# Kernel optimization log

Measured on AMD Instinct MI355X. Metric: run time of the kernel, lower is better.

## Reference

```python
import jax, jax.numpy as jnp
import numpy as np

K = 16
D_MODEL = 128

def _gather(pts, idx):
    # pts: [B,N,C], idx: [B,N,K] -> [B,N,K,C]
    return jax.vmap(lambda p, i: p[i])(pts, idx)

def setup_inputs() -> dict:
    key = jax.random.key(0)
    ks = jax.random.split(key, 20)
    s = 0.05
    def w(k_, shape):
        return jax.random.normal(k_, shape, dtype=jnp.float32) * s
    B, N, C = 4, 4096, 3
    TF, D = 128, D_MODEL
    return {
        "xyz": jax.random.normal(ks[0], (B, N, C), dtype=jnp.float32),
        "W0a": w(ks[1], (C, TF)),  "b0a": jnp.zeros((TF,), jnp.float32),
        "W0b": w(ks[2], (TF, TF)), "b0b": jnp.zeros((TF,), jnp.float32),
        "W1":  w(ks[3], (TF, D)),  "b1":  jnp.zeros((D,), jnp.float32),
        "W2":  w(ks[4], (D, TF)),  "b2":  jnp.zeros((TF,), jnp.float32),
        "Wd1": w(ks[5], (C, D)),   "bd1": jnp.zeros((D,), jnp.float32),
        "Wd2": w(ks[6], (D, D)),   "bd2": jnp.zeros((D,), jnp.float32),
        "Wg1": w(ks[7], (D, D)),   "bg1": jnp.zeros((D,), jnp.float32),
        "Wg2": w(ks[8], (D, D)),   "bg2": jnp.zeros((D,), jnp.float32),
        "Wq":  w(ks[9], (D, D)),
        "Wk":  w(ks[10], (D, D)),
        "Wv":  w(ks[11], (D, D)),
    }

def reference(xyz, W0a, b0a, W0b, b0b, W1, b1, W2, b2,
              Wd1, bd1, Wd2, bd2, Wg1, bg1, Wg2, bg2, Wq, Wk, Wv):
    sq = jnp.sum(xyz * xyz, axis=-1)
    dists = sq[:, :, None] - 2.0 * jnp.einsum('bnc,bmc->bnm', xyz, xyz) + sq[:, None, :]
    _, knn_idx = jax.lax.top_k(-dists, K)          # [B,N,K] nearest neighbors

    knn_xyz = _gather(xyz, knn_idx)                # [B,N,K,3]
    features = jax.nn.relu(xyz @ W0a + b0a) @ W0b + b0b   # fc0  [B,N,TF]
    pre = features
    x = features @ W1 + b1                          # fc1  [B,N,D]
    q = x @ Wq                                      # [B,N,D]
    kf = _gather(x @ Wk, knn_idx)                   # [B,N,K,D]
    vf = _gather(x @ Wv, knn_idx)                   # [B,N,K,D]

    delta = xyz[:, :, None, :] - knn_xyz            # [B,N,K,3]
    pos_enc = jax.nn.relu(delta @ Wd1 + bd1) @ Wd2 + bd2   # fc_delta [B,N,K,D]

    h = q[:, :, None, :] - kf + pos_enc
    attn_logits = jax.nn.relu(h @ Wg1 + bg1) @ Wg2 + bg2   # fc_gamma [B,N,K,D]
    attn = jax.nn.softmax(attn_logits / np.sqrt(D_MODEL).astype(np.float32), axis=-2)

    res = jnp.einsum('bmnf,bmnf->bmf', attn, vf + pos_enc)  # [B,N,D]
    res = res @ W2 + b2 + pre                               # [B,N,TF]
    return res, attn
```

## Files before the change

### kernel.cpp

```cpp
#include <hip/hip_runtime.h>
#include <math.h>

#define BB 4
#define NN 4096
#define KNNK 16
#define DD 128
#define BN (BB*NN)

typedef __attribute__((ext_vector_type(8))) short short8;
typedef __attribute__((ext_vector_type(4))) float floatx4;

__device__ __forceinline__ short f2bf(float x) {
  unsigned u = __float_as_uint(x);
  unsigned r = (u + 0x7fffu + ((u >> 16) & 1u)) >> 16;
  return (short)r;
}

__device__ __forceinline__ float bf2f(short h) {
  return __uint_as_float((unsigned)(unsigned short)h << 16);
}

#define LDSFENCE() asm volatile("s_waitcnt lgkmcnt(0)" ::: "memory")

__device__ __forceinline__ void split_from_lds(const float* __restrict__ trans,
                                               int c, int g, short8 ah[4],
                                               short8 al[4]) {
#pragma unroll
  for (int s = 0; s < 4; ++s) {
    const float* p_ = &trans[c * 132 + s * 32 + g * 8];
    float4 u0 = *reinterpret_cast<const float4*>(p_);
    float4 u1 = *reinterpret_cast<const float4*>(p_ + 4);
    float tmp[8] = {u0.x, u0.y, u0.z, u0.w, u1.x, u1.y, u1.z, u1.w};
#pragma unroll
    for (int j = 0; j < 8; ++j) {
      short h_ = f2bf(tmp[j]);
      ah[s][j] = h_;
      al[s][j] = f2bf(tmp[j] - bf2f(h_));
    }
  }
}

__device__ __forceinline__ void split_gemm2(const short* __restrict__ Bh,
                                            int nt0, int lane,
                                            const short8 ah[4],
                                            const short8 al[4], floatx4& acc0,
                                            floatx4& acc1) {
  const short* Bl = Bh + 16384;
#pragma unroll
  for (int ks = 0; ks < 4; ++ks) {
    const size_t o0 = ((size_t)((nt0 + 0) * 4 + ks) * 64 + lane) * 8;
    const size_t o1 = ((size_t)((nt0 + 1) * 4 + ks) * 64 + lane) * 8;
    short8 bh0 = *reinterpret_cast<const short8*>(Bh + o0);
    short8 bl0 = *reinterpret_cast<const short8*>(Bl + o0);
    short8 bh1 = *reinterpret_cast<const short8*>(Bh + o1);
    short8 bl1 = *reinterpret_cast<const short8*>(Bl + o1);
    acc0 = __builtin_amdgcn_mfma_f32_16x16x32_bf16(ah[ks], bh0, acc0, 0, 0, 0);
    acc1 = __builtin_amdgcn_mfma_f32_16x16x32_bf16(ah[ks], bh1, acc1, 0, 0, 0);
    acc0 = __builtin_amdgcn_mfma_f32_16x16x32_bf16(ah[ks], bl0, acc0, 0, 0, 0);
    acc1 = __builtin_amdgcn_mfma_f32_16x16x32_bf16(ah[ks], bl1, acc1, 0, 0, 0);
    acc0 = __builtin_amdgcn_mfma_f32_16x16x32_bf16(al[ks], bh0, acc0, 0, 0, 0);
    acc1 = __builtin_amdgcn_mfma_f32_16x16x32_bf16(al[ks], bh1, acc1, 0, 0, 0);
  }
}

__device__ __forceinline__ void ced(double& a, double& b) {
  double mn = fmin(a, b);
  double mx = fmax(a, b);
  a = mn;
  b = mx;
}

__device__ __forceinline__ void dsort16(double v[16]) {
#define CE(i, j) ced(v[i], v[j]);
  CE(0, 1) CE(2, 3) CE(4, 5) CE(6, 7) CE(8, 9) CE(10, 11) CE(12, 13) CE(14, 15)
  CE(0, 2) CE(1, 3) CE(4, 6) CE(5, 7) CE(8, 10) CE(9, 11) CE(12, 14) CE(13, 15)
  CE(1, 2) CE(5, 6) CE(9, 10) CE(13, 14)
  CE(0, 4) CE(1, 5) CE(2, 6) CE(3, 7) CE(8, 12) CE(9, 13) CE(10, 14) CE(11, 15)
  CE(2, 4) CE(3, 5) CE(10, 12) CE(11, 13)
  CE(1, 2) CE(3, 4) CE(5, 6) CE(9, 10) CE(11, 12) CE(13, 14)
  CE(0, 8) CE(1, 9) CE(2, 10) CE(3, 11) CE(4, 12) CE(5, 13) CE(6, 14) CE(7, 15)
  CE(4, 8) CE(5, 9) CE(6, 10) CE(7, 11)
  CE(2, 4) CE(3, 5) CE(6, 8) CE(7, 9) CE(10, 12) CE(11, 13)
  CE(1, 2) CE(3, 4) CE(5, 6) CE(7, 8) CE(9, 10) CE(11, 12) CE(13, 14)
#undef CE
}

__device__ __forceinline__ void dbitonic16(double m[16]) {
#pragma unroll
  for (int s = 8; s >= 1; s >>= 1) {
#pragma unroll
    for (int i = 0; i < 16; ++i) {
      if ((i & s) == 0) ced(m[i], m[i + s]);
    }
  }
}

__global__ __launch_bounds__(256, 4) void knn_kernel(const float* __restrict__ xyz,
                                                     int* __restrict__ knn) {
  const int wv = threadIdx.x >> 6;
  const int lane = threadIdx.x & 63;
  const int q = blockIdx.x * 4 + wv;
  const int b = q >> 12;
  const int n = q & 4095;
  const float* xb = xyz + (size_t)b * NN * 3;

  const float qx = xb[n * 3 + 0], qy = xb[n * 3 + 1], qz = xb[n * 3 + 2];
  const float qsq = __fadd_rn(__fadd_rn(__fmul_rn(qx, qx), __fmul_rn(qy, qy)),
                              __fmul_rn(qz, qz));

  double top[16];
#pragma unroll
  for (int batch = 0; batch < 4; ++batch) {
    double v[16];
#pragma unroll
    for (int i = 0; i < 16; ++i) {
      const int c = (batch * 16 + i) * 64 + lane;
      float cx = xb[c * 3 + 0], cy = xb[c * 3 + 1], cz = xb[c * 3 + 2];
      float csq = __fadd_rn(__fadd_rn(__fmul_rn(cx, cx), __fmul_rn(cy, cy)),
                            __fmul_rn(cz, cz));
      float dot = __fadd_rn(__fadd_rn(__fmul_rn(qx, cx), __fmul_rn(qy, cy)),
                            __fmul_rn(qz, cz));
      float d = __fadd_rn(__fsub_rn(qsq, __fmul_rn(2.0f, dot)), csq);
      unsigned u = __float_as_uint(d);
      u = (u & 0x80000000u) ? ~u : (u | 0x80000000u);
      unsigned long long key =
          0x3FF0000000000000ULL | (((unsigned long long)u << 12) | (unsigned)c);
      v[i] = __longlong_as_double((long long)key);
    }
    dsort16(v);
    if (batch == 0) {
#pragma unroll
      for (int i = 0; i < 16; ++i) top[i] = v[i];
    } else {
      double m[16];
#pragma unroll
      for (int i = 0; i < 16; ++i)
        m[i] = fmin(top[i], v[15 - i]);
      dbitonic16(m);
#pragma unroll
      for (int i = 0; i < 16; ++i) top[i] = m[i];
    }
  }

#pragma unroll
  for (int mask = 1; mask <= 32; mask <<= 1) {
    double oth[16];
#pragma unroll
    for (int i = 0; i < 16; ++i) {
      double y = __shfl_xor(top[15 - i], mask);
      oth[i] = fmin(y, top[i]);
    }
    dbitonic16(oth);
#pragma unroll
    for (int i = 0; i < 16; ++i) top[i] = oth[i];
  }

  if (lane == 0) {
    int* outp = knn + (size_t)q * KNNK;
#pragma unroll
    for (int k = 0; k < 16; ++k)
      outp[k] = (int)(__double_as_longlong(top[k]) & 0xFFFLL);
  }
}

__global__ void swz_all_kernel(const float* __restrict__ Wd2,
                               const float* __restrict__ Wg1,
                               const float* __restrict__ Wg2,
                               const float* __restrict__ W0b,
                               const float* __restrict__ W1,
                               const float* __restrict__ Wq,
                               const float* __restrict__ Wk,
                               const float* __restrict__ Wv,
                               const float* __restrict__ W2,
                               short* __restrict__ wsw,
                               short* __restrict__ wsplit) {
  int t = blockIdx.x * 256 + threadIdx.x;
  if (t < 3 * 2048) {
    int stage = t / 2048;
    int rem = t % 2048;
    int nt = rem / 256;
    int ks = (rem % 256) / 64;
    int lane = rem % 64;
    const float* W = (stage == 0) ? Wd2 : (stage == 1) ? Wg1 : Wg2;
    short8 o;
#pragma unroll
    for (int j = 0; j < 8; ++j) {
      int k = ks * 32 + (lane >> 4) * 8 + j;
      int n = nt * 16 + (lane & 15);
      o[j] = f2bf(W[k * 128 + n]);
    }
    *reinterpret_cast<short8*>(wsw + (size_t)t * 8) = o;
  } else {
    int u = t - 3 * 2048;
    if (u >= 6 * 2048) return;
    int mat = u / 2048;
    int rem = u % 2048;
    int nt = rem / 256;
    int ks = (rem % 256) / 64;
    int lane = rem % 64;
    const float* W = (mat == 0) ? W0b : (mat == 1) ? W1 : (mat == 2) ? Wq
                     : (mat == 3) ? Wk : (mat == 4) ? Wv : W2;
    short8 hi, lo;
#pragma unroll
    for (int j = 0; j < 8; ++j) {
      int k = ks * 32 + (lane >> 4) * 8 + j;
      int n = nt * 16 + (lane & 15);
      float w = W[k * 128 + n];
      short h = f2bf(w);
      hi[j] = h;
      lo[j] = f2bf(w - bf2f(h));
    }
    *reinterpret_cast<short8*>(wsplit + ((size_t)(2 * mat) * 2048 + rem) * 8) = hi;
    *reinterpret_cast<short8*>(wsplit + ((size_t)(2 * mat + 1) * 2048 + rem) * 8) = lo;
  }
}

__global__ __launch_bounds__(256, 4) void point_mlp_mfma_kernel(
    const float* __restrict__ xyz, const float* __restrict__ W0a,
    const float* __restrict__ b0a, const float* __restrict__ b0b,
    const float* __restrict__ b1, const short* __restrict__ wsplit,
    float* __restrict__ pre, float* __restrict__ qv, float* __restrict__ kv,
    float* __restrict__ vv) {
  const int wv = threadIdx.x >> 6;
  const int lane = threadIdx.x & 63;
  const int g = lane >> 4;
  const int c = lane & 15;
  const int g0 = blockIdx.x * 16;
  const int nt0 = wv * 2;

  __shared__ __attribute__((aligned(16))) float trans[16 * 132];
  __shared__ float xs[64];
  if (threadIdx.x < 48) {
    int p = threadIdx.x / 3, cc = threadIdx.x % 3;
    xs[p * 4 + cc] = xyz[(size_t)(g0 + p) * 3 + cc];
  }
  __syncthreads();

  short8 ah[4], al[4];
  {
    const float x0 = xs[c * 4 + 0], x1 = xs[c * 4 + 1], x2 = xs[c * 4 + 2];
#pragma unroll
    for (int s = 0; s < 4; ++s) {
#pragma unroll
      for (int j = 0; j < 8; ++j) {
        const int k = s * 32 + g * 8 + j;
        float v = fmaf(x2, W0a[256 + k],
                       fmaf(x1, W0a[128 + k], fmaf(x0, W0a[k], b0a[k])));
        v = fmaxf(v, 0.f);
        const short h = f2bf(v);
        ah[s][j] = h;
        al[s][j] = f2bf(v - bf2f(h));
      }
    }
  }

  floatx4 acc0, acc1;
  const floatx4 zf = (floatx4){0.f, 0.f, 0.f, 0.f};

  acc0 = zf; acc1 = zf;
  split_gemm2(wsplit + 0 * 32768, nt0, lane, ah, al, acc0, acc1);
  {
    const float bb0 = b0b[nt0 * 16 + c];
    const float bb1 = b0b[(nt0 + 1) * 16 + c];
#pragma unroll
    for (int r = 0; r < 4; ++r) {
      const int row = g * 4 + r;
      float v0 = acc0[r] + bb0;
      float v1 = acc1[r] + bb1;
      pre[(size_t)(g0 + row) * 128 + nt0 * 16 + c] = v0;
      pre[(size_t)(g0 + row) * 128 + (nt0 + 1) * 16 + c] = v1;
      trans[row * 132 + nt0 * 16 + c] = v0;
      trans[row * 132 + (nt0 + 1) * 16 + c] = v1;
    }
  }
  __syncthreads();
  split_from_lds(trans, c, g, ah, al);
  __syncthreads();

  acc0 = zf; acc1 = zf;
  split_gemm2(wsplit + 1 * 32768, nt0, lane, ah, al, acc0, acc1);
  {
    const float bb0 = b1[nt0 * 16 + c];
    const float bb1 = b1[(nt0 + 1) * 16 + c];
#pragma unroll
    for (int r = 0; r < 4; ++r) {
      const int row = g * 4 + r;
      trans[row * 132 + nt0 * 16 + c] = acc0[r] + bb0;
      trans[row * 132 + (nt0 + 1) * 16 + c] = acc1[r] + bb1;
    }
  }
  __syncthreads();
  split_from_lds(trans, c, g, ah, al);
  __syncthreads();

#define GSTORE(dst)                                                            \
  _Pragma("unroll") for (int r = 0; r < 4; ++r) {                              \
    const int row = g0 + g * 4 + r;                                            \
    dst[(size_t)row * 128 + nt0 * 16 + c] = acc0[r];                           \
    dst[(size_t)row * 128 + (nt0 + 1) * 16 + c] = acc1[r];                     \
  }

  acc0 = zf; acc1 = zf;
  split_gemm2(wsplit + 2 * 32768, nt0, lane, ah, al, acc0, acc1);
  GSTORE(qv);

  acc0 = zf; acc1 = zf;
  split_gemm2(wsplit + 3 * 32768, nt0, lane, ah, al, acc0, acc1);
  GSTORE(kv);

  acc0 = zf; acc1 = zf;
  split_gemm2(wsplit + 4 * 32768, nt0, lane, ah, al, acc0, acc1);
  GSTORE(vv);

#undef GSTORE
}

__device__ __forceinline__ void wstage(const short* __restrict__ wsw_stage,
                                       short* __restrict__ wlds, int wv,
                                       int lane) {
#pragma unroll
  for (int i = 0; i < 8; ++i) {
    short8 w_ = *reinterpret_cast<const short8*>(wsw_stage + wv * 4096 +
                                                 i * 512 + lane * 8);
    *reinterpret_cast<short8*>(&wlds[wv * 4096 + i * 512 + lane * 8]) = w_;
  }
}

__global__ __launch_bounds__(256, 3) void attn_mfma_kernel(
    const float* __restrict__ xyz, const int* __restrict__ knn,
    const float* __restrict__ qv, const float* __restrict__ kv,
    const float* __restrict__ vv, const short* __restrict__ wsw,
    const float* __restrict__ Wd1, const float* __restrict__ bd1,
    const float* __restrict__ bd2, const float* __restrict__ bg1,
    const float* __restrict__ bg2, float* __restrict__ res_ws,
    float* __restrict__ out_attn) {
  const int wv = threadIdx.x >> 6;
  const int lane = threadIdx.x & 63;
  const int g = lane >> 4;
  const int c = lane & 15;
  const int bn = blockIdx.x * 4 + wv;
  const int b = bn >> 12;
  const int base_n = b << 12;

  __shared__ __attribute__((aligned(16))) short wlds[16384];
  __shared__ __attribute__((aligned(16))) short conv[4][16 * 136];

  const int* knnp = knn + (size_t)bn * 16;
  const int idxn = knnp[c];
  int idxr[4];
#pragma unroll
  for (int r = 0; r < 4; ++r) idxr[r] = knnp[g * 4 + r];

  float kvf[8][4];
#pragma unroll
  for (int nt = 0; nt < 8; ++nt)
#pragma unroll
    for (int r = 0; r < 4; ++r)
      kvf[nt][r] = kv[((size_t)(base_n + idxr[r])) * 128 + nt * 16 + c];

  const float ddx = xyz[(size_t)bn * 3 + 0] - xyz[((size_t)(base_n + idxn)) * 3 + 0];
  const float ddy = xyz[(size_t)bn * 3 + 1] - xyz[((size_t)(base_n + idxn)) * 3 + 1];
  const float ddz = xyz[(size_t)bn * 3 + 2] - xyz[((size_t)(base_n + idxn)) * 3 + 2];

  short8 af[4];
#pragma unroll
  for (int s = 0; s < 4; ++s) {
#pragma unroll
    for (int j = 0; j < 8; ++j) {
      int d = s * 32 + g * 8 + j;
      float v = fmaf(ddz, Wd1[256 + d],
                     fmaf(ddy, Wd1[128 + d], fmaf(ddx, Wd1[d], bd1[d])));
      af[s][j] = f2bf(fmaxf(v, 0.f));
    }
  }

  float qc[8], bd2v[8];
#pragma unroll
  for (int nt = 0; nt < 8; ++nt) {
    qc[nt] = qv[(size_t)bn * 128 + nt * 16 + c];
    bd2v[nt] = bd2[nt * 16 + c];
  }

  floatx4 acc[8];

#define STAGE_GEMM_LDS()                                                       \
  {                                                                            \
    _Pragma("unroll") for (int ks = 0; ks < 4; ++ks) {                         \
      _Pragma("unroll") for (int h2 = 0; h2 < 2; ++h2) {                       \
        short8 bfr[4];                                                         \
        _Pragma("unroll") for (int i = 0; i < 4; ++i)                          \
          bfr[i] = *reinterpret_cast<const short8*>(                           \
              &wlds[((h2 * 4 + i) * 4 + ks) * 512 + lane * 8]);                \
        _Pragma("unroll") for (int i = 0; i < 4; ++i)                          \
          acc[h2 * 4 + i] = __builtin_amdgcn_mfma_f32_16x16x32_bf16(           \
              af[ks], bfr[i], acc[h2 * 4 + i], 0, 0, 0);                       \
      }                                                                        \
    }                                                                          \
  }

  wstage(wsw, wlds, wv, lane);
  __syncthreads();
#pragma unroll
  for (int nt = 0; nt < 8; ++nt) acc[nt] = (floatx4){0.f, 0.f, 0.f, 0.f};
  STAGE_GEMM_LDS();

  float PE[8][4];
#pragma unroll
  for (int nt = 0; nt < 8; ++nt) {
#pragma unroll
    for (int r = 0; r < 4; ++r) {
      float pe = acc[nt][r] + bd2v[nt];
      PE[nt][r] = pe;
      conv[wv][(g * 4 + r) * 136 + nt * 16 + c] =
          f2bf(qc[nt] - kvf[nt][r] + pe);
    }
  }
  LDSFENCE();
#pragma unroll
  for (int s = 0; s < 4; ++s)
    af[s] = *reinterpret_cast<const short8*>(&conv[wv][c * 136 + s * 32 + g * 8]);

  __syncthreads();
  wstage(wsw + 16384, wlds, wv, lane);
  __syncthreads();
#pragma unroll
  for (int nt = 0; nt < 8; ++nt) acc[nt] = (floatx4){0.f, 0.f, 0.f, 0.f};
  STAGE_GEMM_LDS();
#pragma unroll
  for (int nt = 0; nt < 8; ++nt) {
    const float bg1v = bg1[nt * 16 + c];
#pragma unroll
    for (int r = 0; r < 4; ++r) {
      conv[wv][(g * 4 + r) * 136 + nt * 16 + c] =
          f2bf(fmaxf(acc[nt][r] + bg1v, 0.f));
    }
  }
  LDSFENCE();
#pragma unroll
  for (int s = 0; s < 4; ++s)
    af[s] = *reinterpret_cast<const short8*>(&conv[wv][c * 136 + s * 32 + g * 8]);

  __syncthreads();
  wstage(wsw + 32768, wlds, wv, lane);
  __syncthreads();

  const float inv = 0.0883883476483184f;
  float resv[8];
#pragma unroll
  for (int h = 0; h < 2; ++h) {
    const int ntb = h * 4;
    float vvf[4][4];
#pragma unroll
    for (int i = 0; i < 4; ++i)
#pragma unroll
      for (int r = 0; r < 4; ++r)
        vvf[i][r] =
            vv[((size_t)(base_n + idxr[r])) * 128 + (ntb + i) * 16 + c];

    floatx4 acch[4];
#pragma unroll
    for (int i = 0; i < 4; ++i) acch[i] = (floatx4){0.f, 0.f, 0.f, 0.f};
#pragma unroll
    for (int ks = 0; ks < 4; ++ks) {
      short8 bfr[4];
#pragma unroll
      for (int i = 0; i < 4; ++i)
        bfr[i] = *reinterpret_cast<const short8*>(
            &wlds[((ntb + i) * 4 + ks) * 512 + lane * 8]);
#pragma unroll
      for (int i = 0; i < 4; ++i)
        acch[i] = __builtin_amdgcn_mfma_f32_16x16x32_bf16(af[ks], bfr[i],
                                                          acch[i], 0, 0, 0);
    }

#pragma unroll
    for (int i = 0; i < 4; ++i) {
      const int nt = ntb + i;
      const float bg2v = bg2[nt * 16 + c];
      float l0 = (acch[i][0] + bg2v) * inv;
      float l1 = (acch[i][1] + bg2v) * inv;
      float l2 = (acch[i][2] + bg2v) * inv;
      float l3 = (acch[i][3] + bg2v) * inv;
      float m4 = fmaxf(fmaxf(l0, l1), fmaxf(l2, l3));
      m4 = fmaxf(m4, __shfl_xor(m4, 16));
      m4 = fmaxf(m4, __shfl_xor(m4, 32));
      float e0 = expf(l0 - m4), e1 = expf(l1 - m4);
      float e2 = expf(l2 - m4), e3 = expf(l3 - m4);
      float s4 = e0 + e1 + e2 + e3;
      s4 += __shfl_xor(s4, 16);
      s4 += __shfl_xor(s4, 32);
      float rs = 1.f / s4;
      float a0 = e0 * rs, a1 = e1 * rs, a2 = e2 * rs, a3 = e3 * rs;
      size_t base = ((size_t)bn * 16 + g * 4) * 128 + nt * 16 + c;
      out_attn[base + 0 * 128] = a0;
      out_attn[base + 1 * 128] = a1;
      out_attn[base + 2 * 128] = a2;
      out_attn[base + 3 * 128] = a3;
      float r = 0.f;
      r = fmaf(a0, vvf[i][0] + PE[nt][0], r);
      r = fmaf(a1, vvf[i][1] + PE[nt][1], r);
      r = fmaf(a2, vvf[i][2] + PE[nt][2], r);
      r = fmaf(a3, vvf[i][3] + PE[nt][3], r);
      r += __shfl_xor(r, 16);
      r += __shfl_xor(r, 32);
      resv[nt] = r;
    }
  }
#undef STAGE_GEMM_LDS

  if (g == 0) {
#pragma unroll
    for (int nt = 0; nt < 8; ++nt)
      res_ws[(size_t)bn * 128 + nt * 16 + c] = resv[nt];
  }
}

__global__ __launch_bounds__(256, 4) void epilogue_mfma_kernel(
    const float* __restrict__ res_ws, const short* __restrict__ wsplit,
    const float* __restrict__ b2, const float* __restrict__ pre,
    float* __restrict__ out_res) {
  const int wv = threadIdx.x >> 6;
  const int lane = threadIdx.x & 63;
  const int g = lane >> 4;
  const int c = lane & 15;
  const int g0 = blockIdx.x * 16;
  const int nt0 = wv * 2;

  __shared__ __attribute__((aligned(16))) float trans[16 * 132];

#pragma unroll
  for (int i = 0; i < 2; ++i) {
    int idx4 = threadIdx.x + i * 256;
    int row = idx4 >> 5;
    int col4 = idx4 & 31;
    float4 v = *reinterpret_cast<const float4*>(
        res_ws + (size_t)(g0 + row) * 128 + col4 * 4);
    *reinterpret_cast<float4*>(&trans[row * 132 + col4 * 4]) = v;
  }
  __syncthreads();

  short8 ah[4], al[4];
  split_from_lds(trans, c, g, ah, al);

  float prv0[4], prv1[4];
  const float bb0 = b2[nt0 * 16 + c];
  const float bb1 = b2[(nt0 + 1) * 16 + c];
#pragma unroll
  for (int r = 0; r < 4; ++r) {
    prv0[r] = pre[(size_t)(g0 + g * 4 + r) * 128 + nt0 * 16 + c];
    prv1[r] = pre[(size_t)(g0 + g * 4 + r) * 128 + (nt0 + 1) * 16 + c];
  }

  floatx4 acc0 = (floatx4){0.f, 0.f, 0.f, 0.f};
  floatx4 acc1 = (floatx4){0.f, 0.f, 0.f, 0.f};
  split_gemm2(wsplit + 5 * 32768, nt0, lane, ah, al, acc0, acc1);

#pragma unroll
  for (int r = 0; r < 4; ++r) {
    const int row = g0 + g * 4 + r;
    out_res[(size_t)row * 128 + nt0 * 16 + c] = acc0[r] + bb0 + prv0[r];
    out_res[(size_t)row * 128 + (nt0 + 1) * 16 + c] = acc1[r] + bb1 + prv1[r];
  }
}

extern "C" void kernel_launch(void* const* d_in, const int* in_sizes, int n_in,
                              void* d_out, int out_size, void* d_ws,
                              size_t ws_size, hipStream_t stream) {
  const float* xyz = (const float*)d_in[0];
  const float* W0a = (const float*)d_in[1];
  const float* b0a = (const float*)d_in[2];
  const float* W0b = (const float*)d_in[3];
  const float* b0b = (const float*)d_in[4];
  const float* W1 = (const float*)d_in[5];
  const float* b1 = (const float*)d_in[6];
  const float* W2 = (const float*)d_in[7];
  const float* b2 = (const float*)d_in[8];
  const float* Wd1 = (const float*)d_in[9];
  const float* bd1 = (const float*)d_in[10];
  const float* Wd2 = (const float*)d_in[11];
  const float* bd2 = (const float*)d_in[12];
  const float* Wg1 = (const float*)d_in[13];
  const float* bg1 = (const float*)d_in[14];
  const float* Wg2 = (const float*)d_in[15];
  const float* bg2 = (const float*)d_in[16];
  const float* Wq = (const float*)d_in[17];
  const float* Wk = (const float*)d_in[18];
  const float* Wv = (const float*)d_in[19];

  char* ws = (char*)d_ws;
  int* knn = (int*)ws;
  float* pre = (float*)(ws + (1 << 20));
  float* qv = (float*)(ws + (9 << 20));
  float* kv = (float*)(ws + (17 << 20));
  float* vv = (float*)(ws + (25 << 20));
  float* res_ws = (float*)(ws + (33 << 20));
  short* wsw = (short*)(ws + (41 << 20));
  short* wsplit = (short*)(ws + (41 << 20) + (128 << 10));

  float* out_res = (float*)d_out;
  float* out_attn = out_res + (size_t)BN * DD;

  hipLaunchKernelGGL(swz_all_kernel, dim3(72), dim3(256), 0, stream, Wd2, Wg1,
                     Wg2, W0b, W1, Wq, Wk, Wv, W2, wsw, wsplit);
  hipLaunchKernelGGL(knn_kernel, dim3(4096), dim3(256), 0, stream, xyz, knn);
  hipLaunchKernelGGL(point_mlp_mfma_kernel, dim3(1024), dim3(256), 0, stream,
                     xyz, W0a, b0a, b0b, b1, wsplit, pre, qv, kv, vv);
  hipLaunchKernelGGL(attn_mfma_kernel, dim3(4096), dim3(256), 0, stream, xyz,
                     knn, qv, kv, vv, wsw, Wd1, bd1, bd2, bg1, bg2, res_ws,
                     out_attn);
  hipLaunchKernelGGL(epilogue_mfma_kernel, dim3(1024), dim3(256), 0, stream,
                     res_ws, wsplit, b2, pre, out_res);
}
```

Before: 352.6 us.

## Process four kNN queries per wavefront with sixteen lanes each

Remaps the kNN kernel so each wavefront handles four queries, each using 16 lanes that scan 256 candidates apiece in a non-unrolled 16-batch loop. This cuts the cross-lane shuffle-merge stages from six to four per query and shrinks the grid by four. The trade is a longer serial per-lane sort/merge loop and more loop-carried state per thread.

After: 345.9 us. No clear change (-1.9%).

```diff
diff --git a/kernel.cpp b/kernel.cpp
--- a/kernel.cpp
+++ b/kernel.cpp
@@ -99,7 +99,9 @@
                                                      int* __restrict__ knn) {
   const int wv = threadIdx.x >> 6;
   const int lane = threadIdx.x & 63;
-  const int q = blockIdx.x * 4 + wv;
+  const int ln = lane & 15;
+  const int qg = lane >> 4;
+  const int q = blockIdx.x * 16 + wv * 4 + qg;
   const int b = q >> 12;
   const int n = q & 4095;
   const float* xb = xyz + (size_t)b * NN * 3;
@@ -108,42 +110,47 @@
   const float qsq = __fadd_rn(__fadd_rn(__fmul_rn(qx, qx), __fmul_rn(qy, qy)),
                               __fmul_rn(qz, qz));
 
+#define LOADBATCH(batch)                                                       \
+  _Pragma("unroll") for (int i = 0; i < 16; ++i) {                             \
+    const int c = ((batch) * 16 + i) * 16 + ln;                                \
+    float cx = xb[c * 3 + 0], cy = xb[c * 3 + 1], cz = xb[c * 3 + 2];          \
+    float csq = __fadd_rn(__fadd_rn(__fmul_rn(cx, cx), __fmul_rn(cy, cy)),     \
+                          __fmul_rn(cz, cz));                                  \
+    float dot = __fadd_rn(__fadd_rn(__fmul_rn(qx, cx), __fmul_rn(qy, cy)),     \
+                          __fmul_rn(qz, cz));                                  \
+    float d = __fadd_rn(__fsub_rn(qsq, __fmul_rn(2.0f, dot)), csq);            \
+    unsigned u = __float_as_uint(d);                                           \
+    u = (u & 0x80000000u) ? ~u : (u | 0x80000000u);                            \
+    unsigned long long key =                                                   \
+        0x3FF0000000000000ULL | (((unsigned long long)u << 12) | (unsigned)c); \
+    v[i] = __longlong_as_double((long long)key);                               \
+  }
+
   double top[16];
-#pragma unroll
-  for (int batch = 0; batch < 4; ++batch) {
+  {
     double v[16];
-#pragma unroll
-    for (int i = 0; i < 16; ++i) {
-      const int c = (batch * 16 + i) * 64 + lane;
-      float cx = xb[c * 3 + 0], cy = xb[c * 3 + 1], cz = xb[c * 3 + 2];
-      float csq = __fadd_rn(__fadd_rn(__fmul_rn(cx, cx), __fmul_rn(cy, cy)),
-                            __fmul_rn(cz, cz));
-      float dot = __fadd_rn(__fadd_rn(__fmul_rn(qx, cx), __fmul_rn(qy, cy)),
-                            __fmul_rn(qz, cz));
-      float d = __fadd_rn(__fsub_rn(qsq, __fmul_rn(2.0f, dot)), csq);
-      unsigned u = __float_as_uint(d);
-      u = (u & 0x80000000u) ? ~u : (u | 0x80000000u);
-      unsigned long long key =
-          0x3FF0000000000000ULL | (((unsigned long long)u << 12) | (unsigned)c);
-      v[i] = __longlong_as_double((long long)key);
-    }
+    LOADBATCH(0);
     dsort16(v);
-    if (batch == 0) {
-#pragma unroll
-      for (int i = 0; i < 16; ++i) top[i] = v[i];
-    } else {
-      double m[16];
-#pragma unroll
-      for (int i = 0; i < 16; ++i)
-        m[i] = fmin(top[i], v[15 - i]);
-      dbitonic16(m);
-#pragma unroll
-      for (int i = 0; i < 16; ++i) top[i] = m[i];
-    }
-  }
-
-#pragma unroll
-  for (int mask = 1; mask <= 32; mask <<= 1) {
+#pragma unroll
+    for (int i = 0; i < 16; ++i) top[i] = v[i];
+  }
+#pragma unroll 1
+  for (int batch = 1; batch < 16; ++batch) {
+    double v[16];
+    LOADBATCH(batch);
+    dsort16(v);
+    double m[16];
+#pragma unroll
+    for (int i = 0; i < 16; ++i)
+      m[i] = fmin(top[i], v[15 - i]);
+    dbitonic16(m);
+#pragma unroll
+    for (int i = 0; i < 16; ++i) top[i] = m[i];
+  }
+#undef LOADBATCH
+
+#pragma unroll
+  for (int mask = 1; mask <= 8; mask <<= 1) {
     double oth[16];
 #pragma unroll
     for (int i = 0; i < 16; ++i) {
@@ -155,7 +162,7 @@
     for (int i = 0; i < 16; ++i) top[i] = oth[i];
   }
 
-  if (lane == 0) {
+  if (ln == 0) {
     int* outp = knn + (size_t)q * KNNK;
 #pragma unroll
     for (int k = 0; k < 16; ++k)
@@ -602,7 +609,7 @@
 
   hipLaunchKernelGGL(swz_all_kernel, dim3(72), dim3(256), 0, stream, Wd2, Wg1,
                      Wg2, W0b, W1, Wq, Wk, Wv, W2, wsw, wsplit);
-  hipLaunchKernelGGL(knn_kernel, dim3(4096), dim3(256), 0, stream, xyz, knn);
+  hipLaunchKernelGGL(knn_kernel, dim3(1024), dim3(256), 0, stream, xyz, knn);
   hipLaunchKernelGGL(point_mlp_mfma_kernel, dim3(1024), dim3(256), 0, stream,
                      xyz, W0a, b0a, b0b, b1, wsplit, pre, qv, kv, vv);
   hipLaunchKernelGGL(attn_mfma_kernel, dim3(4096), dim3(256), 0, stream, xyz,
```
